# Performance work log

Hardware: AMD Instinct MI355X
Metric: run time of the kernel (lower is better)

The kernel has to match this reference:

```python
import jax, jax.numpy as jnp
import numpy as np

TIMESTEPS = 1000


def setup_inputs() -> dict:
    key = jax.random.key(0)
    k1, k2 = jax.random.split(key)
    rec = jax.random.uniform(k1, (64, 1, 256, 256), dtype=jnp.float32)
    tgt = jax.random.uniform(k2, (64, 1, 256, 256), dtype=jnp.float32)
    return {"reconstructed_image": rec, "target_image": tgt}


def _holographic_transform(img):
    # img: [B, 1, H, W] -> out: [B, 1, H, TIMESTEPS]
    # Original: for every nonzero pixel (x, y) with value v, writes
    #   out[b, 0, x, int(v * timesteps) - 1] = y
    # iterating in row-major (y ascending) order, so for duplicate targets the
    B, C, H, W = img.shape
    x = img[:, 0]  # [B, H, W]
    q = (x * TIMESTEPS).astype(jnp.int32) - 1
    # torch negative indexing wraps (q = -1 -> timesteps - 1); zero pixels are
    # skipped, so route them to an out-of-range index and drop.
    q = jnp.where(x != 0, q % TIMESTEPS, TIMESTEPS)  # [B, H, W]
    y_vals = jnp.broadcast_to(jnp.arange(W, dtype=img.dtype), (B, H, W))
    b_idx = jnp.arange(B)[:, None, None]
    h_idx = jnp.arange(H)[None, :, None]
    out = jnp.zeros((B, 1, H, TIMESTEPS), dtype=img.dtype)
    out = out.at[b_idx, 0, h_idx, q].max(y_vals, mode="drop")
    return out


def reference(reconstructed_image, target_image):
    rec_holo = _holographic_transform(reconstructed_image)
    tgt_holo = _holographic_transform(target_image)
    return jnp.mean((rec_holo - tgt_holo) ** 2)
```

## Files before the change

kernel.cpp:

```cpp
#include <hip/hip_runtime.h>

#define TIMESTEPS 1000
#define NROWS 16384
#define ROWS_PER_WAVE 4
#define WAVES_PER_BLOCK 4
#define NBLOCKS (NROWS / (ROWS_PER_WAVE * WAVES_PER_BLOCK))
#define TOTAL_ELEMS 16384000.0

__global__ __launch_bounds__(256) void holo_row_loss(
    const float* __restrict__ rec,
    const float* __restrict__ tgt,
    double* __restrict__ block_partials)
{
    __shared__ int bins[WAVES_PER_BLOCK][2048];
    __shared__ float wave_sums[WAVES_PER_BLOCK];

    const int tid  = threadIdx.x;
    const int wav  = tid >> 6;
    const int lane = tid & 63;
    const int gw   = blockIdx.x * WAVES_PER_BLOCK + wav;

    int* __restrict__ binw = &bins[wav][0];

    int4 z4; z4.x = 0; z4.y = 0; z4.z = 0; z4.w = 0;
    int4* zb = (int4*)binw;
#pragma unroll
    for (int j = 0; j < 8; ++j) zb[j * 64 + lane] = z4;

    const float4* rec4 = (const float4*)rec;
    const float4* tgt4 = (const float4*)tgt;
    float4 xr[ROWS_PER_WAVE], xt[ROWS_PER_WAVE];
#pragma unroll
    for (int r = 0; r < ROWS_PER_WAVE; ++r) {
        const int row = gw * ROWS_PER_WAVE + r;
        xr[r] = rec4[row * 64 + lane];
        xt[r] = tgt4[row * 64 + lane];
    }
    __builtin_amdgcn_wave_barrier();

    float s = 0.0f;

#pragma unroll
    for (int r = 0; r < ROWS_PER_WAVE; ++r) {
        const int base = (r + 1) << 8;

#pragma unroll
        for (int j = 0; j < 4; ++j) {
            const float vr = (&xr[r].x)[j];
            const float vt = (&xt[r].x)[j];
            const int   w  = lane * 4 + j;
            int q = (int)(vr * 1000.0f) - 1;
            if (q < 0) q += TIMESTEPS;
            if (vr != 0.0f) atomicMax(&binw[q], base | w);
            q = (int)(vt * 1000.0f) - 1;
            if (q < 0) q += TIMESTEPS;
            if (vt != 0.0f) atomicMax(&binw[1024 + q], base | w);
        }
        __builtin_amdgcn_wave_barrier();

        const int4* r4 = (const int4*)binw;
        const int4* t4 = (const int4*)(binw + 1024);
#pragma unroll
        for (int k = 0; k < 4; ++k) {
            const int4 a = r4[k * 64 + lane];
            const int4 b = t4[k * 64 + lane];
            const int wa0 = max(a.x - base, 0), wb0 = max(b.x - base, 0);
            const int wa1 = max(a.y - base, 0), wb1 = max(b.y - base, 0);
            const int wa2 = max(a.z - base, 0), wb2 = max(b.z - base, 0);
            const int wa3 = max(a.w - base, 0), wb3 = max(b.w - base, 0);
            const float d0 = (float)(wa0 - wb0);
            const float d1 = (float)(wa1 - wb1);
            const float d2 = (float)(wa2 - wb2);
            const float d3 = (float)(wa3 - wb3);
            s = fmaf(d0, d0, s);
            s = fmaf(d1, d1, s);
            s = fmaf(d2, d2, s);
            s = fmaf(d3, d3, s);
        }
        __builtin_amdgcn_wave_barrier();
    }

    for (int off = 32; off > 0; off >>= 1) s += __shfl_down(s, off, 64);
    if (lane == 0) wave_sums[wav] = s;
    __syncthreads();
    if (tid == 0) {
        double bsum = (double)wave_sums[0] + (double)wave_sums[1]
                    + (double)wave_sums[2] + (double)wave_sums[3];
        block_partials[blockIdx.x] = bsum;
    }
}

__global__ __launch_bounds__(256) void reduce_partials(
    const double* __restrict__ block_partials,
    float* __restrict__ out)
{
    __shared__ double wave_sums[4];
    const int tid = threadIdx.x;
    double s = 0.0;
#pragma unroll
    for (int i = 0; i < NBLOCKS / 256; ++i)
        s += block_partials[i * 256 + tid];
    for (int off = 32; off > 0; off >>= 1) s += __shfl_down(s, off, 64);
    if ((tid & 63) == 0) wave_sums[tid >> 6] = s;
    __syncthreads();
    if (tid == 0) {
        double tot = wave_sums[0] + wave_sums[1] + wave_sums[2] + wave_sums[3];
        out[0] = (float)(tot / TOTAL_ELEMS);
    }
}

extern "C" void kernel_launch(void* const* d_in, const int* in_sizes, int n_in,
                              void* d_out, int out_size, void* d_ws, size_t ws_size,
                              hipStream_t stream)
{
    const float* rec = (const float*)d_in[0];
    const float* tgt = (const float*)d_in[1];
    float* out = (float*)d_out;
    double* block_partials = (double*)d_ws;

    holo_row_loss<<<NBLOCKS, 256, 0, stream>>>(rec, tgt, block_partials);
    reduce_partials<<<1, 256, 0, stream>>>(block_partials, out);
}
```

Baseline: 77.25 us.

## Halve per-wave LDS bins by sequencing rec/tgt scatters and use integer accumulation

Each wave now uses a single 1024-entry LDS bin array instead of separate rec and tgt arrays. It scatters rec, reads the result into registers, then scatters tgt into the same bins, using increasing base tags so that entries from earlier passes read as empty without re-zeroing. Rows per wave drop from four to two, which doubles the block count, and the second row's loads are issued later to overlap with the first row's work. Loss accumulation switches to exact integer arithmetic. The scatter phases become more serialized and the wr array adds register pressure, in exchange for less LDS per block and higher occupancy.

```diff
diff --git a/kernel.cpp b/kernel.cpp
--- a/kernel.cpp
+++ b/kernel.cpp
@@ -2,18 +2,32 @@
 
 #define TIMESTEPS 1000
 #define NROWS 16384
-#define ROWS_PER_WAVE 4
+#define ROWS_PER_WAVE 2
 #define WAVES_PER_BLOCK 4
 #define NBLOCKS (NROWS / (ROWS_PER_WAVE * WAVES_PER_BLOCK))
 #define TOTAL_ELEMS 16384000.0
 
-__global__ __launch_bounds__(256) void holo_row_loss(
+
+__device__ __forceinline__ void scatter_row(
+    int* __restrict__ binw, const float4& x, int base, int lane)
+{
+#pragma unroll
+    for (int j = 0; j < 4; ++j) {
+        const float v = (&x.x)[j];
+        const int   w = lane * 4 + j;
+        int q = (int)(v * 1000.0f) - 1;
+        if (q < 0) q += TIMESTEPS;
+        if (v != 0.0f) atomicMax(&binw[q], base | w);
+    }
+}
+
+__global__ __launch_bounds__(256, 8) void holo_row_loss(
     const float* __restrict__ rec,
     const float* __restrict__ tgt,
     double* __restrict__ block_partials)
 {
-    __shared__ int bins[WAVES_PER_BLOCK][2048];
-    __shared__ float wave_sums[WAVES_PER_BLOCK];
+    __shared__ int bins[WAVES_PER_BLOCK][1024];
+    __shared__ int wave_sums[WAVES_PER_BLOCK];
 
     const int tid  = threadIdx.x;
     const int wav  = tid >> 6;
@@ -21,72 +35,87 @@
     const int gw   = blockIdx.x * WAVES_PER_BLOCK + wav;
 
     int* __restrict__ binw = &bins[wav][0];
+    const int4* __restrict__ bin4 = (const int4*)binw;
 
     int4 z4; z4.x = 0; z4.y = 0; z4.z = 0; z4.w = 0;
     int4* zb = (int4*)binw;
 #pragma unroll
-    for (int j = 0; j < 8; ++j) zb[j * 64 + lane] = z4;
+    for (int j = 0; j < 4; ++j) zb[j * 64 + lane] = z4;
 
     const float4* rec4 = (const float4*)rec;
     const float4* tgt4 = (const float4*)tgt;
-    float4 xr[ROWS_PER_WAVE], xt[ROWS_PER_WAVE];
+    const int row0 = gw * ROWS_PER_WAVE;
+
+    const float4 xr0 = rec4[row0 * 64 + lane];
+    const float4 xt0 = tgt4[row0 * 64 + lane];
+    __builtin_amdgcn_wave_barrier();
+
+    int s = 0;
+    int wr[16];
+
+    scatter_row(binw, xr0, 1 << 8, lane);
+    __builtin_amdgcn_wave_barrier();
+
+    const float4 xr1 = rec4[(row0 + 1) * 64 + lane];
+    const float4 xt1 = tgt4[(row0 + 1) * 64 + lane];
+
 #pragma unroll
-    for (int r = 0; r < ROWS_PER_WAVE; ++r) {
-        const int row = gw * ROWS_PER_WAVE + r;
-        xr[r] = rec4[row * 64 + lane];
-        xt[r] = tgt4[row * 64 + lane];
+    for (int k = 0; k < 4; ++k) {
+        const int4 a = bin4[k * 64 + lane];
+        wr[k * 4 + 0] = max(a.x - (1 << 8), 0);
+        wr[k * 4 + 1] = max(a.y - (1 << 8), 0);
+        wr[k * 4 + 2] = max(a.z - (1 << 8), 0);
+        wr[k * 4 + 3] = max(a.w - (1 << 8), 0);
     }
     __builtin_amdgcn_wave_barrier();
 
-    float s = 0.0f;
+    scatter_row(binw, xt0, 2 << 8, lane);
+    __builtin_amdgcn_wave_barrier();
 
 #pragma unroll
-    for (int r = 0; r < ROWS_PER_WAVE; ++r) {
-        const int base = (r + 1) << 8;
+    for (int k = 0; k < 4; ++k) {
+        const int4 b = bin4[k * 64 + lane];
+        const int d0 = wr[k * 4 + 0] - max(b.x - (2 << 8), 0);
+        const int d1 = wr[k * 4 + 1] - max(b.y - (2 << 8), 0);
+        const int d2 = wr[k * 4 + 2] - max(b.z - (2 << 8), 0);
+        const int d3 = wr[k * 4 + 3] - max(b.w - (2 << 8), 0);
+        s += d0 * d0; s += d1 * d1; s += d2 * d2; s += d3 * d3;
+    }
+    __builtin_amdgcn_wave_barrier();
+
+    scatter_row(binw, xr1, 3 << 8, lane);
+    __builtin_amdgcn_wave_barrier();
 
 #pragma unroll
-        for (int j = 0; j < 4; ++j) {
-            const float vr = (&xr[r].x)[j];
-            const float vt = (&xt[r].x)[j];
-            const int   w  = lane * 4 + j;
-            int q = (int)(vr * 1000.0f) - 1;
-            if (q < 0) q += TIMESTEPS;
-            if (vr != 0.0f) atomicMax(&binw[q], base | w);
-            q = (int)(vt * 1000.0f) - 1;
-            if (q < 0) q += TIMESTEPS;
-            if (vt != 0.0f) atomicMax(&binw[1024 + q], base | w);
-        }
-        __builtin_amdgcn_wave_barrier();
+    for (int k = 0; k < 4; ++k) {
+        const int4 a = bin4[k * 64 + lane];
+        wr[k * 4 + 0] = max(a.x - (3 << 8), 0);
+        wr[k * 4 + 1] = max(a.y - (3 << 8), 0);
+        wr[k * 4 + 2] = max(a.z - (3 << 8), 0);
+        wr[k * 4 + 3] = max(a.w - (3 << 8), 0);
+    }
+    __builtin_amdgcn_wave_barrier();
 
-        const int4* r4 = (const int4*)binw;
-        const int4* t4 = (const int4*)(binw + 1024);
+    scatter_row(binw, xt1, 4 << 8, lane);
+    __builtin_amdgcn_wave_barrier();
+
 #pragma unroll
-        for (int k = 0; k < 4; ++k) {
-            const int4 a = r4[k * 64 + lane];
-            const int4 b = t4[k * 64 + lane];
-            const int wa0 = max(a.x - base, 0), wb0 = max(b.x - base, 0);
-            const int wa1 = max(a.y - base, 0), wb1 = max(b.y - base, 0);
-            const int wa2 = max(a.z - base, 0), wb2 = max(b.z - base, 0);
-            const int wa3 = max(a.w - base, 0), wb3 = max(b.w - base, 0);
-            const float d0 = (float)(wa0 - wb0);
-            const float d1 = (float)(wa1 - wb1);
-            const float d2 = (float)(wa2 - wb2);
-            const float d3 = (float)(wa3 - wb3);
-            s = fmaf(d0, d0, s);
-            s = fmaf(d1, d1, s);
-            s = fmaf(d2, d2, s);
-            s = fmaf(d3, d3, s);
-        }
-        __builtin_amdgcn_wave_barrier();
+    for (int k = 0; k < 4; ++k) {
+        const int4 b = bin4[k * 64 + lane];
+        const int d0 = wr[k * 4 + 0] - max(b.x - (4 << 8), 0);
+        const int d1 = wr[k * 4 + 1] - max(b.y - (4 << 8), 0);
+        const int d2 = wr[k * 4 + 2] - max(b.z - (4 << 8), 0);
+        const int d3 = wr[k * 4 + 3] - max(b.w - (4 << 8), 0);
+        s += d0 * d0; s += d1 * d1; s += d2 * d2; s += d3 * d3;
     }
 
     for (int off = 32; off > 0; off >>= 1) s += __shfl_down(s, off, 64);
     if (lane == 0) wave_sums[wav] = s;
     __syncthreads();
     if (tid == 0) {
-        double bsum = (double)wave_sums[0] + (double)wave_sums[1]
-                    + (double)wave_sums[2] + (double)wave_sums[3];
-        block_partials[blockIdx.x] = bsum;
+        const long long bsum = (long long)wave_sums[0] + wave_sums[1]
+                             + (long long)wave_sums[2] + wave_sums[3];
+        block_partials[blockIdx.x] = (double)bsum;
     }
 }
 
```

Result: no change. 77.59 us (+0.4%).
